# Kernel optimization log

Measured on AMD Instinct MI355X. Metric: run time of the kernel, lower is better.

## Reference

```python
import jax, jax.numpy as jnp
import numpy as np

B, L, HSIZE = 16, 512, 1024
H, D = 16, 64  # HHEAD = HSIZE/base, HBASE = 64

def setup_inputs() -> dict:
    key = jax.random.key(0)
    ks = jax.random.split(key, 10)
    inp = {
        'v': jax.random.normal(ks[0], (B, L, HSIZE), jnp.float32),
        'k': jax.random.normal(ks[1], (B, L, HSIZE), jnp.float32),
        'q': jax.random.normal(ks[2], (B, L, HSIZE), jnp.float32),
        'img_abs': jax.random.normal(ks[3], (B, L, HSIZE), jnp.float32),
        'Wv': jax.random.normal(ks[4], (HSIZE, HSIZE), jnp.float32) * 0.02,
        'Wk': jax.random.normal(ks[5], (HSIZE, HSIZE), jnp.float32) * 0.02,
        'Wq': jax.random.normal(ks[6], (HSIZE, HSIZE), jnp.float32) * 0.02,
        'Wm': jax.random.normal(ks[7], (HSIZE, HSIZE), jnp.float32) * 0.02,
        'abs_mask': jax.random.bernoulli(ks[8], 0.1, (B, 1, L, L)),
        'mask': jax.random.bernoulli(ks[9], 0.1, (B, 1, L, L)),
    }
    return inp

def reference(v, k, q, img_abs, Wv, Wk, Wq, Wm, abs_mask, mask):
    nb = q.shape[0]
    # Linear (no bias) then split heads: [B, L, HSIZE] -> [B, H, L, D]
    def heads(x):
        return x.reshape(nb, -1, H, D).transpose(0, 2, 1, 3)
    vh = heads(v @ Wv.T)
    kh = heads(k @ Wk.T)
    qh = heads(q @ Wq.T)
    ph = heads(img_abs)
    scale = 1.0 / jnp.sqrt(jnp.asarray(D, qh.dtype))
    # modulate: attention of q over positional features, residual-added to q
    s1 = jnp.einsum('bhqd,bhpd->bhqp', qh, ph) * scale
    s1 = jnp.where(abs_mask, jnp.asarray(-1e9, s1.dtype), s1)
    qh = qh + jnp.einsum('bhqp,bhpd->bhqd', jax.nn.softmax(s1, axis=-1), ph)
    # main attention (dropout = identity in eval mode)
    s2 = jnp.einsum('bhqd,bhkd->bhqk', qh, kh) * scale
    s2 = jnp.where(mask, jnp.asarray(-1e9, s2.dtype), s2)
    atted = jnp.einsum('bhqk,bhkd->bhqd', jax.nn.softmax(s2, axis=-1), vh)
    atted = atted.transpose(0, 2, 1, 3).reshape(nb, -1, H * D)
    return atted @ Wm.T
```

## Files before the change

kernel.cpp:

```cpp
#include <hip/hip_runtime.h>

typedef unsigned short u16;
typedef unsigned int u32;
typedef unsigned long long u64;
typedef __attribute__((ext_vector_type(8))) short short8;
typedef __attribute__((ext_vector_type(4))) float f32x4;
typedef __attribute__((ext_vector_type(4))) u32 u32x4;

#define NB 16
#define SL 512
#define HS 1024
#define NHEAD 16
#define HD 64
#define NTOKC (16L * 512 * 1024)
#define NWC   (1024L * 1024)
#define NMC   (16L * 512 * 512)

typedef const __attribute__((address_space(1))) u32* gas_t;
typedef __attribute__((address_space(3))) u32* las_t;

__device__ __forceinline__ void gld16(const u16* g, u16* l) {
  __builtin_amdgcn_global_load_lds((gas_t)g, (las_t)l, 16, 0, 0);
}

__device__ __forceinline__ u16 f2bf(float f) {
  union { float f; unsigned u; } c; c.f = f;
  unsigned r = c.u + 0x7FFFu + ((c.u >> 16) & 1u);
  return (u16)(r >> 16);
}
__device__ __forceinline__ float bf2f(u16 u) {
  union { float f; unsigned u; } c; c.u = ((unsigned)u) << 16;
  return c.f;
}
__device__ __forceinline__ u32 cvt_pk_bf16(float a, float b) {
  u32 r;
  asm("v_cvt_pk_bf16_f32 %0, %1, %2" : "=v"(r) : "v"(a), "v"(b));
  return r;
}

__global__ __launch_bounds__(256) void prep(
    const float* __restrict__ v, const float* __restrict__ k,
    const float* __restrict__ q, const float* __restrict__ img,
    const float* __restrict__ Wv, const float* __restrict__ Wk,
    const float* __restrict__ Wq, const float* __restrict__ Wm,
    const int* __restrict__ absm, const int* __restrict__ mask,
    u16* __restrict__ ovk, u16* __restrict__ xq, u16* __restrict__ pb,
    u16* __restrict__ w4, u64* __restrict__ bits) {
  const int y = blockIdx.y;
  const long bx = blockIdx.x;
  if (y < 4) {
    const float* in = y == 0 ? v : y == 1 ? k : y == 2 ? q : img;
    u16* out = y == 0 ? ovk : y == 1 ? ovk + NTOKC : y == 2 ? xq : pb;
    long i = (bx * 256 + threadIdx.x) * 4;
    float4 f = *(const float4*)(in + i);
    uint2 u;
    u.x = (unsigned)f2bf(f.x) | ((unsigned)f2bf(f.y) << 16);
    u.y = (unsigned)f2bf(f.z) | ((unsigned)f2bf(f.w) << 16);
    *(uint2*)(out + i) = u;
  } else if (y == 4) {
    if (bx >= 4096) return;
    long i = bx * 1024 + threadIdx.x * 4;
    int j = (int)(i >> 20);
    const float* in = j == 0 ? Wv : j == 1 ? Wk : j == 2 ? Wq : Wm;
    long off = i & (NWC - 1);
    float4 f = *(const float4*)(in + off);
    uint2 u;
    u.x = (unsigned)f2bf(f.x) | ((unsigned)f2bf(f.y) << 16);
    u.y = (unsigned)f2bf(f.z) | ((unsigned)f2bf(f.w) << 16);
    *(uint2*)(w4 + i) = u;
  } else {
#pragma unroll
    for (int rep = 0; rep < 4; ++rep) {
      long i = (bx * 4 + rep) * 256 + threadIdx.x;
      const int* m = (i >= NMC) ? mask : absm;
      long off = i & (NMC - 1);
      u64 bset = __ballot(m[off] != 0);
      if ((threadIdx.x & 63) == 0) bits[i >> 6] = bset;
    }
  }
}

__global__ __launch_bounds__(256) void gemm_p3(const u16* __restrict__ Avk,
                                               const u16* __restrict__ Aq,
                                               const u16* __restrict__ W4,
                                               u16* __restrict__ Cb) {
  __shared__ u16 As[128 * 64];
  __shared__ u16 Bs[128 * 64];
  const int tid = threadIdx.x;
  const int wave = tid >> 6, lane = tid & 63;
  const int quad = lane >> 4, l16 = lane & 15;
  const int l7 = l16 & 7;
  const int sel = blockIdx.x >> 6;
  const int row0 = (blockIdx.x & 63) * 128, col0 = blockIdx.y * 128;
  const int wm = (wave >> 1) * 64, wn = (wave & 1) * 64;
  const int lrow = lane >> 3;
  const int scb = (lane & 7) ^ lrow;
  const int K = HS, N = HS;

  const u16* A = (sel == 2) ? Aq : Avk + (long)sel * NTOKC;
  const u16* W = W4 + (long)sel * NWC;
  u16* C = Cb + (long)sel * NTOKC;

  f32x4 acc[4][4];
#pragma unroll
  for (int mt = 0; mt < 4; ++mt)
#pragma unroll
    for (int nt = 0; nt < 4; ++nt) acc[mt][nt] = (f32x4){0.f, 0.f, 0.f, 0.f};

  const u16* Ab = A + (long)row0 * K;
  const u16* Wb = W + (long)col0 * K;

  for (int k0 = 0; k0 < K; k0 += 64) {
    __syncthreads();
#pragma unroll
    for (int it = 0; it < 4; ++it) {
      int seg = wave * 4 + it;
      int r = seg * 8 + lrow;
      gld16(Ab + (long)r * K + k0 + scb * 8, As + seg * 512);
      gld16(Wb + (long)r * K + k0 + scb * 8, Bs + seg * 512);
    }
    __syncthreads();
#pragma unroll
    for (int kt = 0; kt < 2; ++kt) {
      short8 af[4], bw[4];
#pragma unroll
      for (int mt = 0; mt < 4; ++mt)
        af[mt] = *(const short8*)(As + (wm + mt * 16 + l16) * 64 +
                                  (((kt * 4 + quad) ^ l7) * 8));
#pragma unroll
      for (int nt = 0; nt < 4; ++nt)
        bw[nt] = *(const short8*)(Bs + (wn + nt * 16 + l16) * 64 +
                                  (((kt * 4 + quad) ^ l7) * 8));
#pragma unroll
      for (int mt = 0; mt < 4; ++mt)
#pragma unroll
        for (int nt = 0; nt < 4; ++nt)
          acc[mt][nt] = __builtin_amdgcn_mfma_f32_16x16x32_bf16(
              af[mt], bw[nt], acc[mt][nt], 0, 0, 0);
    }
  }
#pragma unroll
  for (int mt = 0; mt < 4; ++mt)
#pragma unroll
    for (int nt = 0; nt < 4; ++nt)
#pragma unroll
      for (int i = 0; i < 4; ++i) {
        long r = row0 + wm + mt * 16 + quad * 4 + i;
        long c = col0 + wn + nt * 16 + l16;
        C[r * N + c] = f2bf(acc[mt][nt][i]);
      }
}

__global__ __launch_bounds__(256) void gemm_f(const u16* __restrict__ A,
                                              const u16* __restrict__ W,
                                              float* __restrict__ C) {
  __shared__ u16 As[128 * 64];
  __shared__ u16 Bs[128 * 64];
  const int tid = threadIdx.x;
  const int wave = tid >> 6, lane = tid & 63;
  const int quad = lane >> 4, l16 = lane & 15;
  const int l7 = l16 & 7;
  const int row0 = blockIdx.x * 128, col0 = blockIdx.y * 128;
  const int wm = (wave >> 1) * 64, wn = (wave & 1) * 64;
  const int lrow = lane >> 3;
  const int scb = (lane & 7) ^ lrow;
  const int K = HS, N = HS;

  f32x4 acc[4][4];
#pragma unroll
  for (int mt = 0; mt < 4; ++mt)
#pragma unroll
    for (int nt = 0; nt < 4; ++nt) acc[mt][nt] = (f32x4){0.f, 0.f, 0.f, 0.f};

  const u16* Ab = A + (long)row0 * K;
  const u16* Wb = W + (long)col0 * K;

  for (int k0 = 0; k0 < K; k0 += 64) {
    __syncthreads();
#pragma unroll
    for (int it = 0; it < 4; ++it) {
      int seg = wave * 4 + it;
      int r = seg * 8 + lrow;
      gld16(Ab + (long)r * K + k0 + scb * 8, As + seg * 512);
      gld16(Wb + (long)r * K + k0 + scb * 8, Bs + seg * 512);
    }
    __syncthreads();
#pragma unroll
    for (int kt = 0; kt < 2; ++kt) {
      short8 af[4], bw[4];
#pragma unroll
      for (int mt = 0; mt < 4; ++mt)
        af[mt] = *(const short8*)(As + (wm + mt * 16 + l16) * 64 +
                                  (((kt * 4 + quad) ^ l7) * 8));
#pragma unroll
      for (int nt = 0; nt < 4; ++nt)
        bw[nt] = *(const short8*)(Bs + (wn + nt * 16 + l16) * 64 +
                                  (((kt * 4 + quad) ^ l7) * 8));
#pragma unroll
      for (int mt = 0; mt < 4; ++mt)
#pragma unroll
        for (int nt = 0; nt < 4; ++nt)
          acc[mt][nt] = __builtin_amdgcn_mfma_f32_16x16x32_bf16(
              af[mt], bw[nt], acc[mt][nt], 0, 0, 0);
    }
  }
#pragma unroll
  for (int mt = 0; mt < 4; ++mt)
#pragma unroll
    for (int nt = 0; nt < 4; ++nt)
#pragma unroll
      for (int i = 0; i < 4; ++i) {
        long r = row0 + wm + mt * 16 + quad * 4 + i;
        long c = col0 + wn + nt * 16 + l16;
        C[r * N + c] = acc[mt][nt][i];
      }
}

template <bool SAME>
__device__ __forceinline__ void attn_stage(
    const u16* __restrict__ Kb, const u16* __restrict__ Vb,
    const u64* __restrict__ Mb, int qbase, short8 qf[4][2], float l_p[4],
    f32x4 o[4][4], u16 (*Ks)[72], u16 (*Vs)[72],
    int quad, int l16, int sr, int sds, int vcol) {
  uint4 kp = *(const uint4*)(Kb + (long)sr * HS + sds);
  uint4 vp;
  if (!SAME) vp = *(const uint4*)(Vb + (long)sr * HS + sds);
  u64 mcur[4], mnxt[4];
#pragma unroll
  for (int p = 0; p < 4; ++p) mcur[p] = Mb[(long)(qbase + p * 128) * 8];
  {
    *(uint4*)&Ks[sr][sds] = kp;
    union { uint4 q; u16 e[8]; } tv;
    tv.q = SAME ? kp : vp;
#pragma unroll
    for (int j = 0; j < 8; ++j) Vs[sds + j][vcol] = tv.e[j];
  }
  __syncthreads();
  for (int t = 0; t < 8; ++t) {
    const int cur = t & 1;
    if (t < 7) {
      kp = *(const uint4*)(Kb + (long)((t + 1) * 64 + sr) * HS + sds);
      if (!SAME)
        vp = *(const uint4*)(Vb + (long)((t + 1) * 64 + sr) * HS + sds);
#pragma unroll
      for (int p = 0; p < 4; ++p)
        mnxt[p] = Mb[(long)(qbase + p * 128) * 8 + t + 1];
    }
    u16(*Kc)[72] = Ks + cur * 64;
    u16(*Vc)[72] = Vs + cur * 64;
    short8 ak[2][4], bv[2][4];
#pragma unroll
    for (int kt = 0; kt < 2; ++kt)
#pragma unroll
      for (int nt = 0; nt < 4; ++nt) {
        ak[kt][nt] = *(const short8*)&Kc[nt * 16 + l16][kt * 32 + quad * 8];
        bv[kt][nt] = *(const short8*)&Vc[nt * 16 + l16]
                                       [(kt * 32 + quad * 8) ^ ((nt & 3) << 4)];
      }
#pragma unroll
    for (int p = 0; p < 4; ++p) {
      f32x4 s[4];
#pragma unroll
      for (int nt = 0; nt < 4; ++nt) s[nt] = (f32x4){0.f, 0.f, 0.f, 0.f};
#pragma unroll
      for (int kt = 0; kt < 2; ++kt)
#pragma unroll
        for (int nt = 0; nt < 4; ++nt)
          s[nt] = __builtin_amdgcn_mfma_f32_16x16x32_bf16(ak[kt][nt],
                                                          qf[p][kt], s[nt],
                                                          0, 0, 0);
      const u64 mw = mcur[p];
      u32 pk[8];
      float lp = 0.f;
#pragma unroll
      for (int nt = 0; nt < 4; ++nt) {
        const u32 mb = (u32)(mw >> (nt * 16 + quad * 4));
#pragma unroll
        for (int ih = 0; ih < 2; ++ih) {
          float p0 = (mb & (1u << (2 * ih)))
                         ? 0.f
                         : __expf(s[nt][2 * ih] * 0.125f);
          float p1 = (mb & (1u << (2 * ih + 1)))
                         ? 0.f
                         : __expf(s[nt][2 * ih + 1] * 0.125f);
          lp += p0 + p1;
          pk[nt * 2 + ih] = cvt_pk_bf16(p0, p1);
        }
      }
      l_p[p] += lp;
#pragma unroll
      for (int kt = 0; kt < 2; ++kt) {
        u32x4 av;
#pragma unroll
        for (int j2 = 0; j2 < 4; ++j2) {
          int src = ((quad & 1) * 2 + (j2 >> 1)) * 16 + l16;
          u32 vlo = (u32)__shfl((int)pk[(2 * kt) * 2 + (j2 & 1)], src, 64);
          u32 vhi = (u32)__shfl((int)pk[(2 * kt + 1) * 2 + (j2 & 1)], src, 64);
          av[j2] = (quad & 2) ? vhi : vlo;
        }
        union { u32x4 u; short8 s8; } cv;
        cv.u = av;
#pragma unroll
        for (int nt = 0; nt < 4; ++nt)
          o[p][nt] = __builtin_amdgcn_mfma_f32_16x16x32_bf16(
              cv.s8, bv[kt][nt], o[p][nt], 0, 0, 0);
      }
    }
    if (t < 7) {
      u16(*Kn)[72] = Ks + (cur ^ 1) * 64;
      u16(*Vn)[72] = Vs + (cur ^ 1) * 64;
      *(uint4*)&Kn[sr][sds] = kp;
      union { uint4 q; u16 e[8]; } tv;
      tv.q = SAME ? kp : vp;
#pragma unroll
      for (int j = 0; j < 8; ++j) Vn[sds + j][vcol] = tv.e[j];
#pragma unroll
      for (int p = 0; p < 4; ++p) mcur[p] = mnxt[p];
      __syncthreads();
    }
  }
}

__global__ __launch_bounds__(512, 2) void attn_fused(
    const u16* __restrict__ Qp, const u16* __restrict__ Pbp,
    const u16* __restrict__ Kp, const u16* __restrict__ Vp,
    const u64* __restrict__ B0, const u64* __restrict__ B1,
    u16* __restrict__ Op) {
  __shared__ u16 Ks[128][72];
  __shared__ u16 Vs[128][72];
  const int tid = threadIdx.x;
  const int wave = tid >> 6, lane = tid & 63;
  const int quad = lane >> 4, l16 = lane & 15;
  const int h = blockIdx.x, b = blockIdx.y;
  const long bs = (long)SL * HS;
  const u16* Qb = Qp + (long)b * bs + h * HD;
  const u16* Pb = Pbp + (long)b * bs + h * HD;
  const u16* Kb = Kp + (long)b * bs + h * HD;
  const u16* Vb = Vp + (long)b * bs + h * HD;
  const u64* M0 = B0 + (long)b * SL * 8;
  const u64* M1 = B1 + (long)b * SL * 8;
  const int sr = tid >> 3, sds = (tid & 7) * 8;
  const int vcol = sr ^ (((sds >> 4) & 3) << 4);
  const int qbase = wave * 16 + l16;

  short8 qf[4][2];
#pragma unroll
  for (int p = 0; p < 4; ++p)
#pragma unroll
    for (int kt = 0; kt < 2; ++kt)
      qf[p][kt] = *(const short8*)(Qb + (long)(p * 128 + qbase) * HS +
                                   kt * 32 + quad * 8);

  float l_p[4] = {0.f, 0.f, 0.f, 0.f};
  f32x4 o[4][4];
#pragma unroll
  for (int p = 0; p < 4; ++p)
#pragma unroll
    for (int nt = 0; nt < 4; ++nt) o[p][nt] = (f32x4){0.f, 0.f, 0.f, 0.f};

  attn_stage<true>(Pb, Pb, M0, qbase, qf, l_p, o, Ks, Vs, quad, l16, sr, sds,
                   vcol);

  __syncthreads();
#pragma unroll
  for (int p = 0; p < 4; ++p) {
    float rs = l_p[p];
    rs += __shfl_xor(rs, 16, 64);
    rs += __shfl_xor(rs, 32, 64);
    float inv = 1.f / rs;
    float invq[4];
#pragma unroll
    for (int i = 0; i < 4; ++i) invq[i] = __shfl(inv, quad * 4 + i, 64);
#pragma unroll
    for (int i = 0; i < 4; ++i)
#pragma unroll
      for (int nt = 0; nt < 4; ++nt)
        Ks[wave * 16 + quad * 4 + i][nt * 16 + l16] =
            f2bf(o[p][nt][i] * invq[i]);
#pragma unroll
    for (int kt = 0; kt < 2; ++kt) {
      short8 t8 = *(const short8*)&Ks[wave * 16 + l16][kt * 32 + quad * 8];
#pragma unroll
      for (int j = 0; j < 8; ++j)
        qf[p][kt][j] = (short)f2bf(bf2f((u16)t8[j]) + bf2f((u16)qf[p][kt][j]));
    }
#pragma unroll
    for (int nt = 0; nt < 4; ++nt) o[p][nt] = (f32x4){0.f, 0.f, 0.f, 0.f};
    l_p[p] = 0.f;
  }
  __syncthreads();

  attn_stage<false>(Kb, Vb, M1, qbase, qf, l_p, o, Ks, Vs, quad, l16, sr, sds,
                    vcol);

  u16* Ob = Op + (long)b * bs + h * HD;
#pragma unroll
  for (int p = 0; p < 4; ++p) {
    float rs = l_p[p];
    rs += __shfl_xor(rs, 16, 64);
    rs += __shfl_xor(rs, 32, 64);
    float inv = 1.f / rs;
    float invq[4];
#pragma unroll
    for (int i = 0; i < 4; ++i) invq[i] = __shfl(inv, quad * 4 + i, 64);
#pragma unroll
    for (int i = 0; i < 4; ++i) {
      int r = p * 128 + wave * 16 + quad * 4 + i;
#pragma unroll
      for (int nt = 0; nt < 4; ++nt)
        Ob[(long)r * HS + nt * 16 + l16] = f2bf(o[p][nt][i] * invq[i]);
    }
  }
}

extern "C" void kernel_launch(void* const* d_in, const int* in_sizes, int n_in,
                              void* d_out, int out_size, void* d_ws,
                              size_t ws_size, hipStream_t stream) {
  const float* v   = (const float*)d_in[0];
  const float* k   = (const float*)d_in[1];
  const float* q   = (const float*)d_in[2];
  const float* img = (const float*)d_in[3];
  const float* Wv  = (const float*)d_in[4];
  const float* Wk  = (const float*)d_in[5];
  const float* Wq  = (const float*)d_in[6];
  const float* Wm  = (const float*)d_in[7];
  const int* absm  = (const int*)d_in[8];
  const int* mask  = (const int*)d_in[9];
  float* out = (float*)d_out;

  const long NTOK = NTOKC;
  const long NW   = NWC;
  const long NM   = NMC;
  u16* ovk = (u16*)d_out;
  u16* ws  = (u16*)d_ws;
  u16* xq  = ws;
  u16* pb  = ws + 1 * NTOK;
  u16* vh  = ws + 2 * NTOK;
  u16* kh  = ws + 3 * NTOK;
  u16* qh  = ws + 4 * NTOK;
  u16* w4  = ws + 5 * NTOK;
  u64* bt0 = (u64*)(w4 + 4 * NW);
  u64* bt1 = bt0 + NM / 64;
  u16* att = xq;

  prep<<<dim3(8192, 6), 256, 0, stream>>>(v, k, q, img, Wv, Wk, Wq, Wm,
                                          absm, mask, ovk, xq, pb, w4, bt0);
  gemm_p3<<<dim3(192, 8), 256, 0, stream>>>(ovk, xq, w4, vh);
  attn_fused<<<dim3(NHEAD, NB), 512, 0, stream>>>(
      qh, pb, kh, vh, bt0, bt1, att);
  gemm_f<<<dim3(NB * SL / 128, HS / 128), 256, 0, stream>>>(att, w4 + 3 * NW,
                                                            out);
}
```

Before: 371.6 us.

## Split attention query rows across two blocks per head and raise occupancy

```diff
diff --git a/kernel.cpp b/kernel.cpp
--- a/kernel.cpp
+++ b/kernel.cpp
@@ -219,15 +219,15 @@
 template <bool SAME>
 __device__ __forceinline__ void attn_stage(
     const u16* __restrict__ Kb, const u16* __restrict__ Vb,
-    const u64* __restrict__ Mb, int qbase, short8 qf[4][2], float l_p[4],
-    f32x4 o[4][4], u16 (*Ks)[72], u16 (*Vs)[72],
+    const u64* __restrict__ Mb, int qrow0, short8 qf[2][2], float l_p[2],
+    f32x4 o[2][4], u16 (*Ks)[72], u16 (*Vs)[72],
     int quad, int l16, int sr, int sds, int vcol) {
   uint4 kp = *(const uint4*)(Kb + (long)sr * HS + sds);
   uint4 vp;
   if (!SAME) vp = *(const uint4*)(Vb + (long)sr * HS + sds);
-  u64 mcur[4], mnxt[4];
-#pragma unroll
-  for (int p = 0; p < 4; ++p) mcur[p] = Mb[(long)(qbase + p * 128) * 8];
+  u64 mcur[2], mnxt[2];
+#pragma unroll
+  for (int p = 0; p < 2; ++p) mcur[p] = Mb[(long)(qrow0 + p * 128) * 8];
   {
     *(uint4*)&Ks[sr][sds] = kp;
     union { uint4 q; u16 e[8]; } tv;
@@ -243,32 +243,24 @@
       if (!SAME)
         vp = *(const uint4*)(Vb + (long)((t + 1) * 64 + sr) * HS + sds);
 #pragma unroll
-      for (int p = 0; p < 4; ++p)
-        mnxt[p] = Mb[(long)(qbase + p * 128) * 8 + t + 1];
+      for (int p = 0; p < 2; ++p)
+        mnxt[p] = Mb[(long)(qrow0 + p * 128) * 8 + t + 1];
     }
     u16(*Kc)[72] = Ks + cur * 64;
     u16(*Vc)[72] = Vs + cur * 64;
-    short8 ak[2][4], bv[2][4];
-#pragma unroll
-    for (int kt = 0; kt < 2; ++kt)
-#pragma unroll
-      for (int nt = 0; nt < 4; ++nt) {
-        ak[kt][nt] = *(const short8*)&Kc[nt * 16 + l16][kt * 32 + quad * 8];
-        bv[kt][nt] = *(const short8*)&Vc[nt * 16 + l16]
-                                       [(kt * 32 + quad * 8) ^ ((nt & 3) << 4)];
-      }
-#pragma unroll
-    for (int p = 0; p < 4; ++p) {
+#pragma unroll
+    for (int p = 0; p < 2; ++p) {
       f32x4 s[4];
 #pragma unroll
       for (int nt = 0; nt < 4; ++nt) s[nt] = (f32x4){0.f, 0.f, 0.f, 0.f};
 #pragma unroll
       for (int kt = 0; kt < 2; ++kt)
 #pragma unroll
-        for (int nt = 0; nt < 4; ++nt)
-          s[nt] = __builtin_amdgcn_mfma_f32_16x16x32_bf16(ak[kt][nt],
-                                                          qf[p][kt], s[nt],
-                                                          0, 0, 0);
+        for (int nt = 0; nt < 4; ++nt) {
+          short8 ak = *(const short8*)&Kc[nt * 16 + l16][kt * 32 + quad * 8];
+          s[nt] = __builtin_amdgcn_mfma_f32_16x16x32_bf16(ak, qf[p][kt],
+                                                          s[nt], 0, 0, 0);
+        }
       const u64 mw = mcur[p];
       u32 pk[8];
       float lp = 0.f;
@@ -301,9 +293,12 @@
         union { u32x4 u; short8 s8; } cv;
         cv.u = av;
 #pragma unroll
-        for (int nt = 0; nt < 4; ++nt)
+        for (int nt = 0; nt < 4; ++nt) {
+          short8 bv = *(const short8*)&Vc[nt * 16 + l16]
+                                        [(kt * 32 + quad * 8) ^ ((nt & 3) << 4)];
           o[p][nt] = __builtin_amdgcn_mfma_f32_16x16x32_bf16(
-              cv.s8, bv[kt][nt], o[p][nt], 0, 0, 0);
+              cv.s8, bv, o[p][nt], 0, 0, 0);
+        }
       }
     }
     if (t < 7) {
@@ -314,14 +309,14 @@
       tv.q = SAME ? kp : vp;
 #pragma unroll
       for (int j = 0; j < 8; ++j) Vn[sds + j][vcol] = tv.e[j];
-#pragma unroll
-      for (int p = 0; p < 4; ++p) mcur[p] = mnxt[p];
+      mcur[0] = mnxt[0];
+      mcur[1] = mnxt[1];
       __syncthreads();
     }
   }
 }
 
-__global__ __launch_bounds__(512, 2) void attn_fused(
+__global__ __launch_bounds__(512, 4) void attn_fused(
     const u16* __restrict__ Qp, const u16* __restrict__ Pbp,
     const u16* __restrict__ Kp, const u16* __restrict__ Vp,
     const u64* __restrict__ B0, const u64* __restrict__ B1,
@@ -331,7 +326,8 @@
   const int tid = threadIdx.x;
   const int wave = tid >> 6, lane = tid & 63;
   const int quad = lane >> 4, l16 = lane & 15;
-  const int h = blockIdx.x, b = blockIdx.y;
+  const int qt = blockIdx.x, h = blockIdx.y, b = blockIdx.z;
+  const int q0 = qt * 256;
   const long bs = (long)SL * HS;
   const u16* Qb = Qp + (long)b * bs + h * HD;
   const u16* Pb = Pbp + (long)b * bs + h * HD;
@@ -341,29 +337,29 @@
   const u64* M1 = B1 + (long)b * SL * 8;
   const int sr = tid >> 3, sds = (tid & 7) * 8;
   const int vcol = sr ^ (((sds >> 4) & 3) << 4);
-  const int qbase = wave * 16 + l16;
-
-  short8 qf[4][2];
-#pragma unroll
-  for (int p = 0; p < 4; ++p)
+  const int qrow0 = q0 + wave * 16 + l16;
+
+  short8 qf[2][2];
+#pragma unroll
+  for (int p = 0; p < 2; ++p)
 #pragma unroll
     for (int kt = 0; kt < 2; ++kt)
-      qf[p][kt] = *(const short8*)(Qb + (long)(p * 128 + qbase) * HS +
+      qf[p][kt] = *(const short8*)(Qb + (long)(qrow0 + p * 128) * HS +
                                    kt * 32 + quad * 8);
 
-  float l_p[4] = {0.f, 0.f, 0.f, 0.f};
-  f32x4 o[4][4];
-#pragma unroll
-  for (int p = 0; p < 4; ++p)
+  float l_p[2] = {0.f, 0.f};
+  f32x4 o[2][4];
+#pragma unroll
+  for (int p = 0; p < 2; ++p)
 #pragma unroll
     for (int nt = 0; nt < 4; ++nt) o[p][nt] = (f32x4){0.f, 0.f, 0.f, 0.f};
 
-  attn_stage<true>(Pb, Pb, M0, qbase, qf, l_p, o, Ks, Vs, quad, l16, sr, sds,
+  attn_stage<true>(Pb, Pb, M0, qrow0, qf, l_p, o, Ks, Vs, quad, l16, sr, sds,
                    vcol);
 
   __syncthreads();
 #pragma unroll
-  for (int p = 0; p < 4; ++p) {
+  for (int p = 0; p < 2; ++p) {
     float rs = l_p[p];
     rs += __shfl_xor(rs, 16, 64);
     rs += __shfl_xor(rs, 32, 64);
@@ -390,12 +386,12 @@
   }
   __syncthreads();
 
-  attn_stage<false>(Kb, Vb, M1, qbase, qf, l_p, o, Ks, Vs, quad, l16, sr, sds,
+  attn_stage<false>(Kb, Vb, M1, qrow0, qf, l_p, o, Ks, Vs, quad, l16, sr, sds,
                     vcol);
 
   u16* Ob = Op + (long)b * bs + h * HD;
 #pragma unroll
-  for (int p = 0; p < 4; ++p) {
+  for (int p = 0; p < 2; ++p) {
     float rs = l_p[p];
     rs += __shfl_xor(rs, 16, 64);
     rs += __shfl_xor(rs, 32, 64);
@@ -405,7 +401,7 @@
     for (int i = 0; i < 4; ++i) invq[i] = __shfl(inv, quad * 4 + i, 64);
 #pragma unroll
     for (int i = 0; i < 4; ++i) {
-      int r = p * 128 + wave * 16 + quad * 4 + i;
+      int r = q0 + p * 128 + wave * 16 + quad * 4 + i;
 #pragma unroll
       for (int nt = 0; nt < 4; ++nt)
         Ob[(long)r * HS + nt * 16 + l16] = f2bf(o[p][nt][i] * invq[i]);
@@ -446,7 +442,7 @@
   prep<<<dim3(8192, 6), 256, 0, stream>>>(v, k, q, img, Wv, Wk, Wq, Wm,
                                           absm, mask, ovk, xq, pb, w4, bt0);
   gemm_p3<<<dim3(192, 8), 256, 0, stream>>>(ovk, xq, w4, vh);
-  attn_fused<<<dim3(NHEAD, NB), 512, 0, stream>>>(
+  attn_fused<<<dim3(SL / 256, NHEAD, NB), 512, 0, stream>>>(
       qh, pb, kh, vh, bt0, bt1, att);
   gemm_f<<<dim3(NB * SL / 128, HS / 128), 256, 0, stream>>>(att, w4 + 3 * NW,
                                                             out);
```

Result: no change. 376.3 us (+1.2%).
